# Optimization experiments

Measured on AMD Instinct MI355X. Metric: run time of the kernel, lower is better.

The kernel has to match this reference:

```python
import jax, jax.numpy as jnp
import numpy as np

D_MODEL = 1024
NUM_HEADS = 16
D_K = D_MODEL // NUM_HEADS


def setup_inputs() -> dict:
    key = jax.random.key(0)
    ks = jax.random.split(key, 12)
    B, S = 2, 2048
    s = 1.0 / np.sqrt(D_MODEL)
    inp = {
        'q': jax.random.normal(ks[0], (B, S, D_MODEL), jnp.float32),
        'k': jax.random.normal(ks[1], (B, S, D_MODEL), jnp.float32),
        'v': jax.random.normal(ks[2], (B, S, D_MODEL), jnp.float32),
        'mask': jax.random.randint(ks[3], (B, S, S), 0, 2, jnp.int32),
        'Wq_w': jax.random.normal(ks[4], (D_MODEL, D_MODEL), jnp.float32) * s,
        'Wq_b': jnp.zeros((D_MODEL,), jnp.float32),
        'Wk_w': jax.random.normal(ks[5], (D_MODEL, D_MODEL), jnp.float32) * s,
        'Wk_b': jnp.zeros((D_MODEL,), jnp.float32),
        'Wv_w': jax.random.normal(ks[6], (D_MODEL, D_MODEL), jnp.float32) * s,
        'Wv_b': jnp.zeros((D_MODEL,), jnp.float32),
        'Wo_w': jax.random.normal(ks[7], (D_MODEL, D_MODEL), jnp.float32) * s,
        'Wo_b': jnp.zeros((D_MODEL,), jnp.float32),
    }
    return inp


def reference(q, k, v, mask, Wq_w, Wq_b, Wk_w, Wk_b, Wv_w, Wv_b, Wo_w, Wo_b):
    B, Sq, _ = q.shape
    # torch Linear: x @ W.T + b
    qp = (q @ Wq_w.T + Wq_b).reshape(B, Sq, NUM_HEADS, D_K)
    kp = (k @ Wk_w.T + Wk_b).reshape(B, k.shape[1], NUM_HEADS, D_K)
    vp = (v @ Wv_w.T + Wv_b).reshape(B, v.shape[1], NUM_HEADS, D_K)
    # scores: [B, H, Sq, Sk]
    scores = jnp.einsum('bqhd,bkhd->bhqk', qp, kp) / np.sqrt(D_K).astype(np.float32)
    scores = jnp.where(mask[:, None, :, :] == 0, jnp.float32(-10000.0), scores)
    attn = jax.nn.softmax(scores, axis=-1)
    ctx = jnp.einsum('bhqk,bkhd->bqhd', attn, vp).reshape(B, Sq, D_MODEL)
    return ctx @ Wo_w.T + Wo_b
```

## Files before the change

### kernel.cpp

```cpp
#include <hip/hip_runtime.h>

#define DM   1024
#define HN   16
#define DKH  64
#define SEQ  2048
#define BATCH 2

typedef __attribute__((ext_vector_type(8))) __bf16 bf16x8;
typedef __attribute__((ext_vector_type(4))) float  f32x4;
typedef __attribute__((ext_vector_type(16))) float f32x16;
typedef __attribute__((ext_vector_type(2)))  int   i32x2;

#define AS1 __attribute__((address_space(1)))
#define AS3 __attribute__((address_space(3)))
#define GLL(g, l) __builtin_amdgcn_global_load_lds((const AS1 unsigned int*)(const void*)(g), \
                                                   (AS3 unsigned int*)(void*)(l), 16, 0, 0)

__device__ __forceinline__ unsigned short f2bf(float f) {
  union { float f; unsigned u; } v; v.f = f;
  unsigned u = v.u;
  u += 0x7FFFu + ((u >> 16) & 1u);
  return (unsigned short)(u >> 16);
}

__global__ __launch_bounds__(256) void prep_kernel(
    const float* __restrict__ q, const float* __restrict__ k,
    const float* __restrict__ v,
    const float* __restrict__ Wq, const float* __restrict__ Wk,
    const float* __restrict__ Wv, const float* __restrict__ Wo,
    const int* __restrict__ mask,
    unsigned short* __restrict__ q_bf, unsigned short* __restrict__ k_bf,
    unsigned short* __restrict__ v_bf,
    unsigned short* __restrict__ Wq_bf, unsigned short* __restrict__ Wk_bf,
    unsigned short* __restrict__ Wv_bf, unsigned short* __restrict__ Wo_bf,
    unsigned* __restrict__ pkm) {
  const int bid = blockIdx.x;
  if (bid < 12288) {
    int t = bid >> 12, r = bid & 4095;
    const float* in = (t == 0) ? q : (t == 1) ? k : v;
    unsigned short* out = (t == 0) ? q_bf : (t == 1) ? k_bf : v_bf;
    int i = r * 256 + threadIdx.x;
    float4 f = ((const float4*)in)[i];
    ushort4 o;
    o.x = f2bf(f.x); o.y = f2bf(f.y); o.z = f2bf(f.z); o.w = f2bf(f.w);
    ((ushort4*)out)[i] = o;
  } else if (bid < 16384) {
    int b2 = bid - 12288;
    int t = b2 >> 10, r = b2 & 1023;
    const float* in = (t == 0) ? Wq : (t == 1) ? Wk : (t == 2) ? Wv : Wo;
    unsigned short* out = (t == 0) ? Wq_bf : (t == 1) ? Wk_bf : (t == 2) ? Wv_bf : Wo_bf;
    int i = r * 256 + threadIdx.x;
    float4 f = ((const float4*)in)[i];
    ushort4 o;
    o.x = f2bf(f.x); o.y = f2bf(f.y); o.z = f2bf(f.z); o.w = f2bf(f.w);
    ((ushort4*)out)[i] = o;
  } else {
    int W = (bid - 16384) * 256 + threadIdx.x;
    const int4* base = (const int4*)(mask + (size_t)(W >> 6) * SEQ + (size_t)(W & 63) * 32);
    unsigned bits = 0;
#pragma unroll
    for (int g = 0; g < 8; ++g) {
      int4 m = base[g];
      bits |= (unsigned)(m.x != 0) << (4 * g);
      bits |= (unsigned)(m.y != 0) << (4 * g + 1);
      bits |= (unsigned)(m.z != 0) << (4 * g + 2);
      bits |= (unsigned)(m.w != 0) << (4 * g + 3);
    }
    pkm[W] = bits;
  }
}

__device__ __forceinline__ void gemm_core_pipe(
    const unsigned short* __restrict__ A,
    const unsigned short* __restrict__ W,
    unsigned short* lds,
    f32x4 (&acc)[4][4]) {
  const int tid = threadIdx.x;
  const int wave = tid >> 6, lane = tid & 63;
  const int l15 = lane & 15, quad = lane >> 4;
  const int wr = wave >> 1, wc = wave & 1;

  const int rl = lane >> 2;
  const int cg = (lane & 3) ^ (((rl & 3) + ((rl >> 2) & 3)) & 3);
  const unsigned short* ga = A + (size_t)(wave * 32 + rl) * DM + cg * 8;
  const unsigned short* gb = W + (size_t)(wave * 32 + rl) * DM + cg * 8;
  unsigned short* la = lds + wave * 1024;
  unsigned short* lb = lds + 4096 + wave * 1024;

  const int cfr = (quad ^ (((l15 & 3) + ((l15 >> 2) & 3)) & 3)) * 8;

  auto stage = [&](int ki, int sb) {
    const unsigned short* a = ga + ki * 32;
    const unsigned short* b = gb + ki * 32;
    GLL(a, la + sb);                    GLL(a + (size_t)16 * DM, la + sb + 512);
    GLL(b, lb + sb);                    GLL(b + (size_t)16 * DM, lb + sb + 512);
  };
  auto compute = [&](int sb) {
    const unsigned short* Ab = lds + sb;
    const unsigned short* Bb = lds + sb + 4096;
    bf16x8 af[4], bfr[4];
#pragma unroll
    for (int mt = 0; mt < 4; ++mt)
      af[mt] = *(const bf16x8*)(Ab + (size_t)(wr * 64 + mt * 16 + l15) * 32 + cfr);
#pragma unroll
    for (int nt = 0; nt < 4; ++nt)
      bfr[nt] = *(const bf16x8*)(Bb + (size_t)(wc * 64 + nt * 16 + l15) * 32 + cfr);
#pragma unroll
    for (int mt = 0; mt < 4; ++mt)
#pragma unroll
      for (int nt = 0; nt < 4; ++nt)
        acc[mt][nt] = __builtin_amdgcn_mfma_f32_16x16x32_bf16(af[mt], bfr[nt], acc[mt][nt], 0, 0, 0);
  };

  stage(0, 0);
  stage(1, 8192);
  int sb0 = 0, sb1 = 8192, sb2 = 16384;
#pragma unroll 1
  for (int i = 0; i < DM / 32 - 2; ++i) {
    stage(i + 2, sb2);
    asm volatile("s_waitcnt vmcnt(8)\ns_barrier" ::: "memory");
    compute(sb0);
    asm volatile("s_barrier" ::: "memory");
    int t = sb0; sb0 = sb1; sb1 = sb2; sb2 = t;
  }
  asm volatile("s_waitcnt vmcnt(4)\ns_barrier" ::: "memory");
  compute(sb0);
  asm volatile("s_waitcnt vmcnt(0)\ns_barrier" ::: "memory");
  compute(sb1);
}

__global__ __launch_bounds__(256, 3) void gemm_qkv(
    const unsigned short* __restrict__ Aq, const unsigned short* __restrict__ Ak,
    const unsigned short* __restrict__ Av,
    const unsigned short* __restrict__ Wq, const unsigned short* __restrict__ Wk,
    const unsigned short* __restrict__ Wv,
    const float* __restrict__ bq, const float* __restrict__ bk,
    const float* __restrict__ bv,
    unsigned short* __restrict__ oq, unsigned short* __restrict__ ok,
    unsigned short* __restrict__ ovT) {
  const int z = blockIdx.z;
  const unsigned short* A = (z == 0) ? Aq : (z == 1) ? Ak : Av;
  const unsigned short* W = (z == 0) ? Wq : (z == 1) ? Wk : Wv;
  const float* bias = (z == 0) ? bq : (z == 1) ? bk : bv;

  __shared__ __align__(16) unsigned short lds[24576];

  const int bn = blockIdx.x * 128, bm = blockIdx.y * 128;
  f32x4 acc[4][4] = {};
  gemm_core_pipe(A + (size_t)bm * DM, W + (size_t)bn * DM, lds, acc);

  const int tid = threadIdx.x;
  const int wave = tid >> 6, lane = tid & 63;
  const int l15 = lane & 15, quad = lane >> 4;
  const int wr = wave >> 1, wc = wave & 1;

  if (z != 2) {
    const float qs = (z == 0) ? 0.125f * 1.44269504088896f : 1.0f;
    unsigned short* out = (z == 0) ? oq : ok;
#pragma unroll
    for (int mt = 0; mt < 4; ++mt)
#pragma unroll
      for (int nt = 0; nt < 4; ++nt) {
        int col = bn + wc * 64 + nt * 16 + l15;
        float bb = bias[col];
#pragma unroll
        for (int r = 0; r < 4; ++r) {
          int row = bm + wr * 64 + mt * 16 + quad * 4 + r;
          out[(size_t)row * DM + col] = f2bf((acc[mt][nt][r] + bb) * qs);
        }
      }
  } else {
    unsigned short* LT = lds;
    __syncthreads();
#pragma unroll
    for (int mt = 0; mt < 4; ++mt)
#pragma unroll
      for (int nt = 0; nt < 4; ++nt) {
        int c = wc * 64 + nt * 16 + l15;
        float bb = bias[bn + c];
        int t0 = wr * 64 + mt * 16 + quad * 4;
        ushort4 w4;
        w4.x = f2bf(acc[mt][nt][0] + bb);
        w4.y = f2bf(acc[mt][nt][1] + bb);
        w4.z = f2bf(acc[mt][nt][2] + bb);
        w4.w = f2bf(acc[mt][nt][3] + bb);
        *(ushort4*)(LT + (size_t)c * 136 + t0) = w4;
      }
    __syncthreads();
    const int b = bm >> 11, sbase = bm & (SEQ - 1);
#pragma unroll
    for (int j = 0; j < 8; ++j) {
      int c = wave * 32 + (j >> 1) * 8 + (lane >> 3);
      int tk = (j & 1) * 64 + (lane & 7) * 8;
      bf16x8 vv = *(const bf16x8*)(LT + (size_t)c * 136 + tk);
      int C = bn + c;
      int h = C >> 6, dk = C & 63;
      *(bf16x8*)(ovT + ((size_t)((b * HN + h) * DKH + dk)) * SEQ + sbase + tk) = vv;
    }
  }
}

__global__ __launch_bounds__(256, 3) void gemm_wo(
    const unsigned short* __restrict__ A, const unsigned short* __restrict__ W,
    const float* __restrict__ bias, float* __restrict__ out) {
  __shared__ __align__(16) unsigned short lds[24576];

  const int bn = blockIdx.x * 128, bm = blockIdx.y * 128;
  f32x4 acc[4][4] = {};
  gemm_core_pipe(A + (size_t)bm * DM, W + (size_t)bn * DM, lds, acc);

  const int tid = threadIdx.x;
  const int wave = tid >> 6, lane = tid & 63;
  const int l15 = lane & 15, quad = lane >> 4;
  const int wr = wave >> 1, wc = wave & 1;

#pragma unroll
  for (int mt = 0; mt < 4; ++mt)
#pragma unroll
    for (int nt = 0; nt < 4; ++nt) {
      int col = bn + wc * 64 + nt * 16 + l15;
      float bb = bias[col];
#pragma unroll
      for (int r = 0; r < 4; ++r) {
        int row = bm + wr * 64 + mt * 16 + quad * 4 + r;
        out[(size_t)row * DM + col] = acc[mt][nt][r] + bb;
      }
    }
}

__global__ __launch_bounds__(256, 2) void attn_kernel(
    const unsigned short* __restrict__ qp,
    const unsigned short* __restrict__ kp,
    const unsigned short* __restrict__ vpT,
    const unsigned* __restrict__ pk,
    unsigned short* __restrict__ ctx) {
  const int lane = threadIdx.x & 63;
  const int wave = threadIdx.x >> 6;
  const int l31 = lane & 31, hi = lane >> 5, l7 = lane & 7;
  const int bh = blockIdx.x;
  const int b = bh >> 4, h = bh & 15;
  const int qrow = blockIdx.y * 128 + wave * 32 + l31;

  __shared__ __align__(16) unsigned short lds[16384];

  const unsigned short* qb = qp + ((size_t)(b * SEQ + qrow)) * DM + h * DKH + hi * 8;
  bf16x8 qf[4];
#pragma unroll
  for (int kt = 0; kt < 4; ++kt) qf[kt] = *(const bf16x8*)(qb + kt * 16);

  f32x16 o0 = {}, o1 = {}, lacc = {};
  bf16x8 ones;
#pragma unroll
  for (int i = 0; i < 8; ++i) ones[i] = (__bf16)1.0f;

  const int r8 = lane >> 3;
  const int cg = (l7 ^ r8) * 8;
  const unsigned short* kg0 = kp + ((size_t)(b * SEQ + wave * 16 + r8)) * DM + h * DKH + cg;
  const unsigned short* kg1 = kg0 + (size_t)8 * DM;
  const unsigned short* vg0 = vpT + ((size_t)(bh * DKH + wave * 16 + r8)) * SEQ + cg;
  const unsigned short* vg1 = vg0 + (size_t)8 * SEQ;
  unsigned short* lK = lds + wave * 1024;
  unsigned short* lV = lds + 8192 + wave * 1024;

  int roff[4];
#pragma unroll
  for (int x = 0; x < 4; ++x)
    roff[x] = l31 * 64 + (((x * 2 + hi) ^ l7) * 8);

  const unsigned* mb = pk + (size_t)(b * SEQ + qrow) * (SEQ / 32);

  auto make_pa = [&](const f32x16& sc, unsigned bits, bf16x8& paA, bf16x8& paB) {
    float p[16];
#pragma unroll
    for (int r = 0; r < 16; ++r) {
      float e = __builtin_amdgcn_exp2f(sc[r]);
      p[r] = ((bits >> ((r & 3) + 8 * (r >> 2))) & 1u) ? e : 0.0f;
    }
    unsigned X0, X1, Y0, Y1;
    asm("v_cvt_pk_bf16_f32 %0, %1, %2" : "=v"(X0) : "v"(p[0]), "v"(p[1]));
    asm("v_cvt_pk_bf16_f32 %0, %1, %2" : "=v"(X1) : "v"(p[2]), "v"(p[3]));
    asm("v_cvt_pk_bf16_f32 %0, %1, %2" : "=v"(Y0) : "v"(p[4]), "v"(p[5]));
    asm("v_cvt_pk_bf16_f32 %0, %1, %2" : "=v"(Y1) : "v"(p[6]), "v"(p[7]));
    i32x2 s0 = __builtin_amdgcn_permlane32_swap((int)X0, (int)Y0, false, false);
    i32x2 s1 = __builtin_amdgcn_permlane32_swap((int)X1, (int)Y1, false, false);
    union { unsigned u[4]; bf16x8 v; } ua;
    ua.u[0] = (unsigned)s0.x; ua.u[1] = (unsigned)s1.x;
    ua.u[2] = (unsigned)s0.y; ua.u[3] = (unsigned)s1.y;
    paA = ua.v;
    asm("v_cvt_pk_bf16_f32 %0, %1, %2" : "=v"(X0) : "v"(p[8]),  "v"(p[9]));
    asm("v_cvt_pk_bf16_f32 %0, %1, %2" : "=v"(X1) : "v"(p[10]), "v"(p[11]));
    asm("v_cvt_pk_bf16_f32 %0, %1, %2" : "=v"(Y0) : "v"(p[12]), "v"(p[13]));
    asm("v_cvt_pk_bf16_f32 %0, %1, %2" : "=v"(Y1) : "v"(p[14]), "v"(p[15]));
    s0 = __builtin_amdgcn_permlane32_swap((int)X0, (int)Y0, false, false);
    s1 = __builtin_amdgcn_permlane32_swap((int)X1, (int)Y1, false, false);
    union { unsigned u[4]; bf16x8 v; } ub;
    ub.u[0] = (unsigned)s0.x; ub.u[1] = (unsigned)s1.x;
    ub.u[2] = (unsigned)s0.y; ub.u[3] = (unsigned)s1.y;
    paB = ub.v;
  };

  auto compute_tile = [&](int j0, const unsigned short* Kb, const unsigned short* Vb) {
    uint2 mw = *(const uint2*)(mb + (j0 >> 5));
    unsigned bx = mw.x >> (4 * hi);
    unsigned by = mw.y >> (4 * hi);

    f32x16 sc0 = {}, sc1 = {};
#pragma unroll
    for (int kt = 0; kt < 4; ++kt) {
      bf16x8 k0 = *(const bf16x8*)(Kb + roff[kt]);
      bf16x8 k1 = *(const bf16x8*)(Kb + 2048 + roff[kt]);
      sc0 = __builtin_amdgcn_mfma_f32_32x32x16_bf16(k0, qf[kt], sc0, 0, 0, 0);
      sc1 = __builtin_amdgcn_mfma_f32_32x32x16_bf16(k1, qf[kt], sc1, 0, 0, 0);
    }

    bf16x8 pa[4];
    make_pa(sc0, bx, pa[0], pa[1]);
    make_pa(sc1, by, pa[2], pa[3]);

#pragma unroll
    for (int kc = 0; kc < 4; ++kc)
      lacc = __builtin_amdgcn_mfma_f32_32x32x16_bf16(pa[kc], ones, lacc, 0, 0, 0);

#pragma unroll
    for (int kc = 0; kc < 4; ++kc) {
      bf16x8 v0 = *(const bf16x8*)(Vb + roff[kc]);
      bf16x8 v1 = *(const bf16x8*)(Vb + 2048 + roff[kc]);
      o0 = __builtin_amdgcn_mfma_f32_32x32x16_bf16(pa[kc], v0, o0, 0, 0, 0);
      o1 = __builtin_amdgcn_mfma_f32_32x32x16_bf16(pa[kc], v1, o1, 0, 0, 0);
    }
  };

  GLL(kg0, lK);           GLL(kg1, lK + 512);
  GLL(vg0, lV);           GLL(vg1, lV + 512);

#pragma unroll 1
  for (int j0 = 0; j0 < SEQ; j0 += 128) {
    __syncthreads();
    if (j0 + 64 < SEQ) {
      GLL(kg0 + (size_t)(j0 + 64) * DM, lK + 4096);
      GLL(kg1 + (size_t)(j0 + 64) * DM, lK + 4096 + 512);
      GLL(vg0 + (j0 + 64), lV + 4096);
      GLL(vg1 + (j0 + 64), lV + 4096 + 512);
    }
    compute_tile(j0, lds, lds + 8192);

    __syncthreads();
    if (j0 + 128 < SEQ) {
      GLL(kg0 + (size_t)(j0 + 128) * DM, lK);
      GLL(kg1 + (size_t)(j0 + 128) * DM, lK + 512);
      GLL(vg0 + (j0 + 128), lV);
      GLL(vg1 + (j0 + 128), lV + 512);
    }
    compute_tile(j0 + 64, lds + 4096, lds + 12288);
  }

  const int qbase = blockIdx.y * 128 + wave * 32;
#pragma unroll
  for (int r = 0; r < 16; ++r) {
    int qg = qbase + (r & 3) + 8 * (r >> 2) + 4 * hi;
    float inv = 1.0f / lacc[r];
    unsigned short* op = ctx + ((size_t)(b * SEQ + qg)) * DM + h * DKH + l31;
    op[0]  = f2bf(o0[r] * inv);
    op[32] = f2bf(o1[r] * inv);
  }
}

extern "C" void kernel_launch(void* const* d_in, const int* in_sizes, int n_in,
                              void* d_out, int out_size, void* d_ws, size_t ws_size,
                              hipStream_t stream) {
  const float* q    = (const float*)d_in[0];
  const float* k    = (const float*)d_in[1];
  const float* v    = (const float*)d_in[2];
  const int*   mask = (const int*)d_in[3];
  const float* Wq_w = (const float*)d_in[4];
  const float* Wq_b = (const float*)d_in[5];
  const float* Wk_w = (const float*)d_in[6];
  const float* Wk_b = (const float*)d_in[7];
  const float* Wv_w = (const float*)d_in[8];
  const float* Wv_b = (const float*)d_in[9];
  const float* Wo_w = (const float*)d_in[10];
  const float* Wo_b = (const float*)d_in[11];

  char* ws = (char*)d_ws;
  const size_t MB = 1024 * 1024;
  unsigned short* q_bf  = (unsigned short*)(ws + 0 * MB);
  unsigned short* k_bf  = (unsigned short*)(ws + 8 * MB);
  unsigned short* v_bf  = (unsigned short*)(ws + 16 * MB);
  unsigned short* Wq_bf = (unsigned short*)(ws + 24 * MB);
  unsigned short* Wk_bf = (unsigned short*)(ws + 26 * MB);
  unsigned short* Wv_bf = (unsigned short*)(ws + 28 * MB);
  unsigned short* Wo_bf = (unsigned short*)(ws + 30 * MB);
  unsigned short* qp    = (unsigned short*)(ws + 32 * MB);
  unsigned short* kp    = (unsigned short*)(ws + 40 * MB);
  unsigned short* vpT   = (unsigned short*)(ws + 48 * MB);
  unsigned short* ctx   = (unsigned short*)(ws + 56 * MB);
  unsigned* pkm = (unsigned*)d_out;

  const int M = BATCH * SEQ;

  prep_kernel<<<17408, 256, 0, stream>>>(q, k, v, Wq_w, Wk_w, Wv_w, Wo_w, mask,
                                         q_bf, k_bf, v_bf, Wq_bf, Wk_bf, Wv_bf,
                                         Wo_bf, pkm);

  gemm_qkv<<<dim3(DM / 128, M / 128, 3), 256, 0, stream>>>(
      q_bf, k_bf, v_bf, Wq_bf, Wk_bf, Wv_bf, Wq_b, Wk_b, Wv_b, qp, kp, vpT);

  attn_kernel<<<dim3(BATCH * HN, SEQ / 128), 256, 0, stream>>>(qp, kp, vpT, pkm, ctx);

  gemm_wo<<<dim3(DM / 128, M / 128), 256, 0, stream>>>(ctx, Wo_bf, Wo_b, (float*)d_out);
}
```

Measured before the change: 134.4 us.

## Split attention key range across two wave groups and reduce partials through LDS

```diff
diff --git a/kernel.cpp b/kernel.cpp
--- a/kernel.cpp
+++ b/kernel.cpp
@@ -228,7 +228,7 @@
     }
 }
 
-__global__ __launch_bounds__(256, 2) void attn_kernel(
+__global__ __launch_bounds__(512, 4) void attn_kernel(
     const unsigned short* __restrict__ qp,
     const unsigned short* __restrict__ kp,
     const unsigned short* __restrict__ vpT,
@@ -236,12 +236,15 @@
     unsigned short* __restrict__ ctx) {
   const int lane = threadIdx.x & 63;
   const int wave = threadIdx.x >> 6;
+  const int wq = wave & 3, wk = wave >> 2;
   const int l31 = lane & 31, hi = lane >> 5, l7 = lane & 7;
   const int bh = blockIdx.x;
   const int b = bh >> 4, h = bh & 15;
-  const int qrow = blockIdx.y * 128 + wave * 32 + l31;
-
-  __shared__ __align__(16) unsigned short lds[16384];
+  const int qrow = blockIdx.y * 128 + wq * 32 + l31;
+  const int kbase = wk << 10;
+
+  __shared__ __align__(16) unsigned short lds[32768];
+  unsigned short* G = lds + wk * 16384;
 
   const unsigned short* qb = qp + ((size_t)(b * SEQ + qrow)) * DM + h * DKH + hi * 8;
   bf16x8 qf[4];
@@ -255,12 +258,12 @@
 
   const int r8 = lane >> 3;
   const int cg = (l7 ^ r8) * 8;
-  const unsigned short* kg0 = kp + ((size_t)(b * SEQ + wave * 16 + r8)) * DM + h * DKH + cg;
+  const unsigned short* kg0 = kp + ((size_t)(b * SEQ + kbase + wq * 16 + r8)) * DM + h * DKH + cg;
   const unsigned short* kg1 = kg0 + (size_t)8 * DM;
-  const unsigned short* vg0 = vpT + ((size_t)(bh * DKH + wave * 16 + r8)) * SEQ + cg;
+  const unsigned short* vg0 = vpT + ((size_t)(bh * DKH + wq * 16 + r8)) * SEQ + kbase + cg;
   const unsigned short* vg1 = vg0 + (size_t)8 * SEQ;
-  unsigned short* lK = lds + wave * 1024;
-  unsigned short* lV = lds + 8192 + wave * 1024;
+  unsigned short* lK = G + wq * 1024;
+  unsigned short* lV = G + 8192 + wq * 1024;
 
   int roff[4];
 #pragma unroll
@@ -269,13 +272,10 @@
 
   const unsigned* mb = pk + (size_t)(b * SEQ + qrow) * (SEQ / 32);
 
-  auto make_pa = [&](const f32x16& sc, unsigned bits, bf16x8& paA, bf16x8& paB) {
+  auto make_pa = [&](const f32x16& sc, bf16x8& paA, bf16x8& paB) {
     float p[16];
 #pragma unroll
-    for (int r = 0; r < 16; ++r) {
-      float e = __builtin_amdgcn_exp2f(sc[r]);
-      p[r] = ((bits >> ((r & 3) + 8 * (r >> 2))) & 1u) ? e : 0.0f;
-    }
+    for (int r = 0; r < 16; ++r) p[r] = __builtin_amdgcn_exp2f(sc[r]);
     unsigned X0, X1, Y0, Y1;
     asm("v_cvt_pk_bf16_f32 %0, %1, %2" : "=v"(X0) : "v"(p[0]), "v"(p[1]));
     asm("v_cvt_pk_bf16_f32 %0, %1, %2" : "=v"(X1) : "v"(p[2]), "v"(p[3]));
@@ -299,12 +299,19 @@
     paB = ub.v;
   };
 
-  auto compute_tile = [&](int j0, const unsigned short* Kb, const unsigned short* Vb) {
-    uint2 mw = *(const uint2*)(mb + (j0 >> 5));
+  auto compute_tile = [&](int kabs, const unsigned short* Kb, const unsigned short* Vb) {
+    uint2 mw = *(const uint2*)(mb + (kabs >> 5));
     unsigned bx = mw.x >> (4 * hi);
     unsigned by = mw.y >> (4 * hi);
 
-    f32x16 sc0 = {}, sc1 = {};
+    f32x16 sc0, sc1;
+#pragma unroll
+    for (int r = 0; r < 16; ++r) {
+      int n = (r & 3) + 8 * (r >> 2);
+      sc0[r] = ((bx >> n) & 1u) ? 0.0f : -16384.0f;
+      sc1[r] = ((by >> n) & 1u) ? 0.0f : -16384.0f;
+    }
+
 #pragma unroll
     for (int kt = 0; kt < 4; ++kt) {
       bf16x8 k0 = *(const bf16x8*)(Kb + roff[kt]);
@@ -314,8 +321,8 @@
     }
 
     bf16x8 pa[4];
-    make_pa(sc0, bx, pa[0], pa[1]);
-    make_pa(sc1, by, pa[2], pa[3]);
+    make_pa(sc0, pa[0], pa[1]);
+    make_pa(sc1, pa[2], pa[3]);
 
 #pragma unroll
     for (int kc = 0; kc < 4; ++kc)
@@ -334,34 +341,62 @@
   GLL(vg0, lV);           GLL(vg1, lV + 512);
 
 #pragma unroll 1
-  for (int j0 = 0; j0 < SEQ; j0 += 128) {
+  for (int j0 = 0; j0 < 1024; j0 += 128) {
     __syncthreads();
-    if (j0 + 64 < SEQ) {
+    if (j0 + 64 < 1024) {
       GLL(kg0 + (size_t)(j0 + 64) * DM, lK + 4096);
       GLL(kg1 + (size_t)(j0 + 64) * DM, lK + 4096 + 512);
       GLL(vg0 + (j0 + 64), lV + 4096);
       GLL(vg1 + (j0 + 64), lV + 4096 + 512);
     }
-    compute_tile(j0, lds, lds + 8192);
+    compute_tile(kbase + j0, G, G + 8192);
 
     __syncthreads();
-    if (j0 + 128 < SEQ) {
+    if (j0 + 128 < 1024) {
       GLL(kg0 + (size_t)(j0 + 128) * DM, lK);
       GLL(kg1 + (size_t)(j0 + 128) * DM, lK + 512);
       GLL(vg0 + (j0 + 128), lV);
       GLL(vg1 + (j0 + 128), lV + 512);
     }
-    compute_tile(j0 + 64, lds + 4096, lds + 12288);
-  }
-
-  const int qbase = blockIdx.y * 128 + wave * 32;
-#pragma unroll
-  for (int r = 0; r < 16; ++r) {
-    int qg = qbase + (r & 3) + 8 * (r >> 2) + 4 * hi;
-    float inv = 1.0f / lacc[r];
-    unsigned short* op = ctx + ((size_t)(b * SEQ + qg)) * DM + h * DKH + l31;
-    op[0]  = f2bf(o0[r] * inv);
-    op[32] = f2bf(o1[r] * inv);
+    compute_tile(kbase + j0 + 64, G + 4096, G + 12288);
+  }
+
+  __syncthreads();
+  float* cbase = (float*)lds + wq * 3328 + lane * 52;
+  if (wk) {
+#pragma unroll
+    for (int i = 0; i < 4; ++i) {
+      f32x4 a, b2, c;
+#pragma unroll
+      for (int j = 0; j < 4; ++j) {
+        a[j] = o0[4 * i + j]; b2[j] = o1[4 * i + j]; c[j] = lacc[4 * i + j];
+      }
+      *(f32x4*)(cbase + 4 * i)      = a;
+      *(f32x4*)(cbase + 16 + 4 * i) = b2;
+      *(f32x4*)(cbase + 32 + 4 * i) = c;
+    }
+  }
+  __syncthreads();
+  if (!wk) {
+#pragma unroll
+    for (int i = 0; i < 4; ++i) {
+      f32x4 a = *(const f32x4*)(cbase + 4 * i);
+      f32x4 b2 = *(const f32x4*)(cbase + 16 + 4 * i);
+      f32x4 c = *(const f32x4*)(cbase + 32 + 4 * i);
+#pragma unroll
+      for (int j = 0; j < 4; ++j) {
+        o0[4 * i + j] += a[j]; o1[4 * i + j] += b2[j]; lacc[4 * i + j] += c[j];
+      }
+    }
+    const int qbase = blockIdx.y * 128 + wq * 32;
+#pragma unroll
+    for (int r = 0; r < 16; ++r) {
+      int qg = qbase + (r & 3) + 8 * (r >> 2) + 4 * hi;
+      float inv = 1.0f / lacc[r];
+      unsigned short* op = ctx + ((size_t)(b * SEQ + qg)) * DM + h * DKH + l31;
+      op[0]  = f2bf(o0[r] * inv);
+      op[32] = f2bf(o1[r] * inv);
+    }
   }
 }
 
@@ -405,7 +440,7 @@
   gemm_qkv<<<dim3(DM / 128, M / 128, 3), 256, 0, stream>>>(
       q_bf, k_bf, v_bf, Wq_bf, Wk_bf, Wv_bf, Wq_b, Wk_b, Wv_b, qp, kp, vpT);
 
-  attn_kernel<<<dim3(BATCH * HN, SEQ / 128), 256, 0, stream>>>(qp, kp, vpT, pkm, ctx);
+  attn_kernel<<<dim3(BATCH * HN, SEQ / 128), 512, 0, stream>>>(qp, kp, vpT, pkm, ctx);
 
   gemm_wo<<<dim3(DM / 128, M / 128), 256, 0, stream>>>(ctx, Wo_bf, Wo_b, (float*)d_out);
 }
```

Measured after the change: 137.3 us (median of 2 runs). +2.2%, slower.
